# Optimization experiments

Measured on AMD Instinct MI355X. Metric: run time of the kernel, lower is better.

## Reference

```python
import jax, jax.numpy as jnp
import numpy as np

B, N, T = 2, 2048, 2048
ENC, DEC, HID = 1024, 1024, 1024
HEADS = 16
DH = HID // HEADS          # 64
HALF = DH // 2             # 32
LAMBDA_INIT = 0.8


def setup_inputs() -> dict:
    key = jax.random.key(0)
    ks = jax.random.split(key, 9)
    s = 0.02
    return {
        "encoder_feature": jax.random.normal(ks[0], (B, N, ENC), jnp.float32),
        "decoder_feature": jax.random.normal(ks[1], (B, T, DEC), jnp.float32),
        "Wq": jax.random.normal(ks[2], (HID, DEC), jnp.float32) * s,
        "Wk": jax.random.normal(ks[3], (HID, ENC), jnp.float32) * s,
        "Wv": jax.random.normal(ks[4], (HID, ENC), jnp.float32) * s,
        "lambda_q1": jax.random.normal(ks[5], (HALF,), jnp.float32) * 0.1,
        "lambda_q2": jax.random.normal(ks[6], (HALF,), jnp.float32) * 0.1,
        "lambda_k1": jax.random.normal(ks[7], (HALF,), jnp.float32) * 0.1,
        "lambda_k2": jax.random.normal(ks[8], (HALF,), jnp.float32) * 0.1,
    }


def reference(encoder_feature, decoder_feature, Wq, Wk, Wv,
              lambda_q1, lambda_q2, lambda_k1, lambda_k2):
    b, n, _ = encoder_feature.shape
    _, t, _ = decoder_feature.shape
    hid = Wq.shape[0]
    dh = hid // HEADS
    half = dh // 2

    q = decoder_feature @ Wq.T                                # [B,T,hid]
    k = encoder_feature @ Wk.T                                # [B,N,hid]
    v = encoder_feature @ Wv.T                                # [B,N,hid]

    q = q.reshape(b, t, 2 * HEADS, half).transpose(0, 2, 1, 3)  # [B,2H,T,half]
    k = k.reshape(b, n, 2 * HEADS, half).transpose(0, 2, 1, 3)  # [B,2H,N,half]
    v = v.reshape(b, n, HEADS, dh).transpose(0, 2, 1, 3)        # [B,H,N,dh]

    lam = (jnp.exp(jnp.sum(lambda_q1 * lambda_k1))
           - jnp.exp(jnp.sum(lambda_q2 * lambda_k2)) + LAMBDA_INIT)

    scale = 1.0 / jnp.sqrt(jnp.float32(half))
    att = jax.nn.softmax(jnp.einsum('bhtd,bhnd->bhtn', q, k) * scale, axis=-1)
    att = att.reshape(b, HEADS, 2, t, n)
    att = att[:, :, 0] - lam * att[:, :, 1]                   # [B,H,T,N]

    out = jnp.einsum('bhtn,bhnd->bhtd', att, v)               # [B,H,T,dh]
    return out.transpose(0, 2, 1, 3).reshape(b, t, hid)        # dropout: eval no-op
```

## Files before the change

### kernel.cpp

```cpp
#include <hip/hip_runtime.h>

typedef short bf16x8 __attribute__((ext_vector_type(8)));
typedef float f32x4  __attribute__((ext_vector_type(4)));
typedef unsigned int u32x2 __attribute__((ext_vector_type(2)));

#define B_SZ   2
#define T_SZ   2048
#define N_SZ   2048
#define HID_SZ 1024
#define NHEADS 16

#define SLOG2E 0.25500297f

static __device__ __forceinline__ float fexp2(float x) {
#if __has_builtin(__builtin_amdgcn_exp2f)
    return __builtin_amdgcn_exp2f(x);
#else
    float r; __asm__("v_exp_f32 %0, %1" : "=v"(r) : "v"(x)); return r;
#endif
}

static __device__ __forceinline__ short f2bf(float f) {
    unsigned u = __float_as_uint(f);
    u = (u + 0x7fffu + ((u >> 16) & 1u)) >> 16;
    return (short)u;
}

static __device__ __forceinline__ unsigned pk2(float a, float b) {
#if __has_builtin(__builtin_amdgcn_perm)
    return __builtin_amdgcn_perm(__float_as_uint(b) + 0x8000u,
                                 __float_as_uint(a) + 0x8000u, 0x07060302u);
#else
    unsigned ua = (__float_as_uint(a) + 0x8000u) >> 16;
    unsigned ub = (__float_as_uint(b) + 0x8000u) & 0xffff0000u;
    return ua | ub;
#endif
}

static __device__ __forceinline__ void gload16(const void* g, void* l) {
    __builtin_amdgcn_global_load_lds(
        (const __attribute__((address_space(1))) unsigned int*)g,
        (__attribute__((address_space(3))) unsigned int*)l, 16, 0, 0);
}

#define MFMA16(a, b, c) __builtin_amdgcn_mfma_f32_16x16x32_bf16((a), (b), (c), 0, 0, 0)

__global__ __launch_bounds__(256) void cvt_kernel(
    const float* __restrict__ dec, const float* __restrict__ enc,
    const float* __restrict__ Wq, const float* __restrict__ Wk,
    const float* __restrict__ Wv,
    short* __restrict__ decb, short* __restrict__ encb,
    short* __restrict__ wqb, short* __restrict__ wkb, short* __restrict__ wvb)
{
    const float* src; short* dst; int n;
    switch (blockIdx.y) {
      case 0: src = dec; dst = decb; n = B_SZ * T_SZ * HID_SZ; break;
      case 1: src = enc; dst = encb; n = B_SZ * N_SZ * HID_SZ; break;
      case 2: src = Wq;  dst = wqb;  n = HID_SZ * HID_SZ;      break;
      case 3: src = Wk;  dst = wkb;  n = HID_SZ * HID_SZ;      break;
      default:src = Wv;  dst = wvb;  n = HID_SZ * HID_SZ;      break;
    }
    const int idx = (blockIdx.x * 256 + threadIdx.x) * 8;
    if (idx >= n) return;
    float4 a = *(const float4*)&src[idx];
    float4 b = *(const float4*)&src[idx + 4];
    bf16x8 r;
    r[0]=f2bf(a.x); r[1]=f2bf(a.y); r[2]=f2bf(a.z); r[3]=f2bf(a.w);
    r[4]=f2bf(b.x); r[5]=f2bf(b.y); r[6]=f2bf(b.z); r[7]=f2bf(b.w);
    *(bf16x8*)&dst[idx] = r;
}

__global__ __launch_bounds__(256) void proj_kernel(
    const short* __restrict__ decb, const short* __restrict__ encb,
    const short* __restrict__ wqb, const short* __restrict__ wkb,
    const short* __restrict__ wvb,
    short* __restrict__ qbuf, short* __restrict__ kblk, short* __restrict__ vblk)
{
    const int i    = blockIdx.x;
    const int work = (i & 7) * 96 + (i >> 3);
    const int proj = work >> 8;
    const int rem  = work & 255;
    const int c0   = (rem >> 5) * 128;
    const int m0   = (rem & 31) * 128;

    const short* __restrict__ X = (proj == 0) ? decb : encb;
    const short* __restrict__ W = (proj == 0) ? wqb : ((proj == 1) ? wkb : wvb);

    __shared__ short As[128 * 64];
    __shared__ short Bs[128 * 64];

    const int tid  = threadIdx.x;
    const int lane = tid & 63;
    const int w    = tid >> 6;
    const int wm   = (w >> 1) * 64;
    const int wn   = (w & 1) * 64;
    const int q4   = lane >> 4;
    const int r16  = lane & 15;

    const int srow = w * 32;
    const int lrow = lane >> 3;
    const int lxor = (((lane & 7) ^ lrow) * 8);

    f32x4 acc[4][4] = {};

    for (int k0 = 0; k0 < HID_SZ; k0 += 64) {
        __syncthreads();
#pragma unroll
        for (int j = 0; j < 4; ++j) {
            const int row = srow + j * 8 + lrow;
            gload16(&X[(size_t)(m0 + row) * HID_SZ + k0 + lxor],
                    &As[(srow + j * 8) * 64]);
            gload16(&W[(size_t)(c0 + row) * HID_SZ + k0 + lxor],
                    &Bs[(srow + j * 8) * 64]);
        }
        __syncthreads();

#pragma unroll
        for (int kk = 0; kk < 2; ++kk) {
            bf16x8 af[4], bfr[4];
#pragma unroll
            for (int mi = 0; mi < 4; ++mi)
                af[mi] = *(const bf16x8*)&As[(wm + mi * 16 + r16) * 64
                                             + (((kk * 4 + q4) ^ (r16 & 7)) * 8)];
#pragma unroll
            for (int ni = 0; ni < 4; ++ni)
                bfr[ni] = *(const bf16x8*)&Bs[(wn + ni * 16 + r16) * 64
                                              + (((kk * 4 + q4) ^ (r16 & 7)) * 8)];
#pragma unroll
            for (int mi = 0; mi < 4; ++mi)
#pragma unroll
                for (int ni = 0; ni < 4; ++ni)
                    acc[mi][ni] = MFMA16(af[mi], bfr[ni], acc[mi][ni]);
        }
    }

#pragma unroll
    for (int mi = 0; mi < 4; ++mi)
#pragma unroll
    for (int ni = 0; ni < 4; ++ni)
#pragma unroll
    for (int r = 0; r < 4; ++r) {
        const int m = m0 + wm + mi * 16 + q4 * 4 + r;
        const int c = c0 + wn + ni * 16 + r16;
        const float v = acc[mi][ni][r];
        if (proj == 0) {
            qbuf[(size_t)m * HID_SZ + c] = f2bf(v * SLOG2E);
        } else {
            const int bb = m >> 11, n = m & (N_SZ - 1);
            const int hh = c >> 6;
            const int nc = n >> 6;
            const size_t base = ((size_t)((bb * NHEADS + hh) * 32 + nc)) * 4096;
            if (proj == 1) {
                const int row = n & 63, kd = c & 63;
                const int g = kd >> 3, e = kd & 7;
                kblk[base + row * 64 + (((g ^ (row & 7)) << 3) | e)] = f2bf(v);
            } else {
                const int vd = c & 63, nl = n & 63;
                const int np = ((nl & 15) << 2) | ((nl >> 4) & 3);
                const int g = np >> 3, e = np & 7;
                vblk[base + vd * 64 + (((g ^ (vd & 7)) << 3) | e)] = f2bf(v);
            }
        }
    }
}

__global__ __launch_bounds__(256) void attn_kernel(
    const short* __restrict__ qbuf, const short* __restrict__ kblk,
    const short* __restrict__ vblk,
    const float* __restrict__ lq1, const float* __restrict__ lq2,
    const float* __restrict__ lk1, const float* __restrict__ lk2,
    float* __restrict__ out)
{
    const int bi   = blockIdx.x;
    const int work = (bi & 7) * 128 + (bi >> 3);
    const int t0   = (work & 31) * 64;
    const int hb   = work >> 5;
    const int h    = hb & 15;
    const int b    = hb >> 4;

    const int tid = threadIdx.x;
    const int w    = tid >> 6;
    const int lane = tid & 63;
    const int q4   = lane >> 4;
    const int r16  = lane & 15;

    float d1 = 0.f, d2 = 0.f;
#pragma unroll
    for (int i = 0; i < 32; ++i) { d1 += lq1[i] * lk1[i]; d2 += lq2[i] * lk2[i]; }
    const float lam = __expf(d1) - __expf(d2) + 0.8f;

    __shared__ short Ks[4096];
    __shared__ short Vs[4096];
    __shared__ short Pl[4][2048];
    short* __restrict__ P = &Pl[w][0];

    const int trow = t0 + w * 16 + r16;
    const short* qrow = qbuf + ((size_t)(b * T_SZ + trow)) * HID_SZ + h * 64;
    const bf16x8 aq1 = *(const bf16x8*)(qrow + q4 * 8);
    const bf16x8 aq2 = *(const bf16x8*)(qrow + 32 + q4 * 8);

    const short* kbh = kblk + ((size_t)(b * NHEADS + h)) * 32 * 4096;
    const short* vbh = vblk + ((size_t)(b * NHEADS + h)) * 32 * 4096;

    bf16x8 ones;
#pragma unroll
    for (int i = 0; i < 8; ++i) ones[i] = (short)0x3F80;

    f32x4 o0[4] = {}, o1[4] = {};
    f32x4 l0a = {0.f, 0.f, 0.f, 0.f}, l1a = {0.f, 0.f, 0.f, 0.f};

    const int wg_half = (r16 >> 1);
    const int wlo     = (r16 & 1) * 4;
    const int swz     = r16 & 7;

    for (int nc = 0; nc < 32; ++nc) {
        const short* Kg = kbh + nc * 4096;
        const short* Vg = vbh + nc * 4096;

        __syncthreads();
#pragma unroll
        for (int j = 0; j < 2; ++j) {
            gload16(&Kg[(w * 2 + j) * 512 + lane * 8], &Ks[(w * 2 + j) * 512]);
            gload16(&Vg[(w * 2 + j) * 512 + lane * 8], &Vs[(w * 2 + j) * 512]);
        }
        __syncthreads();

        const f32x4 zz = {0.f, 0.f, 0.f, 0.f};
        f32x4 s0[4], s1[4];
#pragma unroll
        for (int s = 0; s < 4; ++s) {
            const int row = s * 16 + r16;
            bf16x8 bk1 = *(const bf16x8*)&Ks[row * 64 + ((q4 ^ swz) << 3)];
            bf16x8 bk2 = *(const bf16x8*)&Ks[row * 64 + (((4 + q4) ^ swz) << 3)];
            s0[s] = MFMA16(aq1, bk1, zz);
            s1[s] = MFMA16(aq2, bk2, zz);
        }

#pragma unroll
        for (int r = 0; r < 4; ++r) {
            const int row = q4 * 4 + r;
            const int wo  = row * 64 + ((wg_half ^ (row & 7)) << 3) + wlo;
            u32x2 pw;
            pw[0] = pk2(fexp2(s0[0][r]), fexp2(s0[1][r]));
            pw[1] = pk2(fexp2(s0[2][r]), fexp2(s0[3][r]));
            *(u32x2*)&P[wo] = pw;
            pw[0] = pk2(fexp2(s1[0][r]), fexp2(s1[1][r]));
            pw[1] = pk2(fexp2(s1[2][r]), fexp2(s1[3][r]));
            *(u32x2*)&P[1024 + wo] = pw;
        }

#pragma unroll
        for (int kk = 0; kk < 2; ++kk) {
            const int ro = r16 * 64 + (((kk * 4 + q4) ^ swz) << 3);
            bf16x8 ap0 = *(const bf16x8*)&P[ro];
            bf16x8 ap1 = *(const bf16x8*)&P[1024 + ro];
            l0a = MFMA16(ap0, ones, l0a);
            l1a = MFMA16(ap1, ones, l1a);
#pragma unroll
            for (int d = 0; d < 4; ++d) {
                const int vd = d * 16 + r16;
                bf16x8 bv = *(const bf16x8*)&Vs[vd * 64 + (((kk * 4 + q4) ^ swz) << 3)];
                o0[d] = MFMA16(ap0, bv, o0[d]);
                o1[d] = MFMA16(ap1, bv, o1[d]);
            }
        }
    }

    float rl0[4], rl1[4];
#pragma unroll
    for (int r = 0; r < 4; ++r) { rl0[r] = 1.f / l0a[r]; rl1[r] = lam / l1a[r]; }

#pragma unroll
    for (int d = 0; d < 4; ++d)
#pragma unroll
        for (int r = 0; r < 4; ++r) {
            const int t  = t0 + w * 16 + q4 * 4 + r;
            const int vd = d * 16 + r16;
            out[((size_t)(b * T_SZ + t)) * HID_SZ + h * 64 + vd] =
                o0[d][r] * rl0[r] - o1[d][r] * rl1[r];
        }
}

extern "C" void kernel_launch(void* const* d_in, const int* in_sizes, int n_in,
                              void* d_out, int out_size, void* d_ws, size_t ws_size,
                              hipStream_t stream)
{
    (void)in_sizes; (void)n_in; (void)out_size; (void)ws_size;

    const float* enc = (const float*)d_in[0];
    const float* dec = (const float*)d_in[1];
    const float* Wq  = (const float*)d_in[2];
    const float* Wk  = (const float*)d_in[3];
    const float* Wv  = (const float*)d_in[4];
    const float* lq1 = (const float*)d_in[5];
    const float* lq2 = (const float*)d_in[6];
    const float* lk1 = (const float*)d_in[7];
    const float* lk2 = (const float*)d_in[8];
    float* out = (float*)d_out;

    short* qbuf = (short*)d_ws;
    short* kblk = qbuf + (size_t)4096 * 1024;
    short* vblk = kblk + (size_t)4096 * 1024;
    short* decb = vblk + (size_t)4096 * 1024;
    short* encb = decb + (size_t)2 * 2048 * 1024;
    short* wqb  = encb + (size_t)2 * 2048 * 1024;
    short* wkb  = wqb  + (size_t)1024 * 1024;
    short* wvb  = wkb  + (size_t)1024 * 1024;

    cvt_kernel<<<dim3(2048, 5), 256, 0, stream>>>(
        dec, enc, Wq, Wk, Wv, decb, encb, wqb, wkb, wvb);

    proj_kernel<<<768, 256, 0, stream>>>(
        decb, encb, wqb, wkb, wvb, qbuf, kblk, vblk);

    attn_kernel<<<1024, 256, 0, stream>>>(
        qbuf, kblk, vblk, lq1, lq2, lk1, lk2, out);
}
```

Measured before the change: 245.7 us.

## Software-pipeline projection GEMM loads and double-buffer K/V tiles in attention

The projection GEMM now prefetches the next K-slice from global memory into registers while MFMAs run on the current shared tile, then stores it to LDS. The attention kernel double-buffers K/V chunks in shared memory, issuing async loads for chunk nc+1 before computing chunk nc, which drops one barrier per iteration. The P scratch buffer is halved by processing the two softmax halves sequentially and reusing the loaded V fragments. This is meant to hide global-load latency, at the cost of more registers and more LDS for the K/V buffers. One risk: the single barrier at the top of each attention iteration may not guarantee that the async gload16 of chunk nc+1 has landed before the next iteration reads it.

Result: slower. 319.0 us (+29.8%).

```diff
diff --git a/kernel.cpp b/kernel.cpp
--- a/kernel.cpp
+++ b/kernel.cpp
@@ -101,19 +101,40 @@
     const int lrow = lane >> 3;
     const int lxor = (((lane & 7) ^ lrow) * 8);
 
+    size_t gx[4], gw[4];
+    int ldso[4];
+#pragma unroll
+    for (int j = 0; j < 4; ++j) {
+        const int row = srow + j * 8 + lrow;
+        gx[j] = (size_t)(m0 + row) * HID_SZ + lxor;
+        gw[j] = (size_t)(c0 + row) * HID_SZ + lxor;
+        ldso[j] = (srow + j * 8) * 64 + lane * 8;
+    }
+
+    uint4 ra[4], rb[4];
+#pragma unroll
+    for (int j = 0; j < 4; ++j) {
+        ra[j] = *(const uint4*)&X[gx[j]];
+        rb[j] = *(const uint4*)&W[gw[j]];
+    }
+#pragma unroll
+    for (int j = 0; j < 4; ++j) {
+        *(uint4*)&As[ldso[j]] = ra[j];
+        *(uint4*)&Bs[ldso[j]] = rb[j];
+    }
+    __syncthreads();
+
     f32x4 acc[4][4] = {};
 
-    for (int k0 = 0; k0 < HID_SZ; k0 += 64) {
-        __syncthreads();
-#pragma unroll
-        for (int j = 0; j < 4; ++j) {
-            const int row = srow + j * 8 + lrow;
-            gload16(&X[(size_t)(m0 + row) * HID_SZ + k0 + lxor],
-                    &As[(srow + j * 8) * 64]);
-            gload16(&W[(size_t)(c0 + row) * HID_SZ + k0 + lxor],
-                    &Bs[(srow + j * 8) * 64]);
-        }
-        __syncthreads();
+    for (int it = 0; it < 16; ++it) {
+        if (it < 15) {
+            const int k1 = (it + 1) * 64;
+#pragma unroll
+            for (int j = 0; j < 4; ++j) {
+                ra[j] = *(const uint4*)&X[gx[j] + k1];
+                rb[j] = *(const uint4*)&W[gw[j] + k1];
+            }
+        }
 
 #pragma unroll
         for (int kk = 0; kk < 2; ++kk) {
@@ -131,6 +152,16 @@
 #pragma unroll
                 for (int ni = 0; ni < 4; ++ni)
                     acc[mi][ni] = MFMA16(af[mi], bfr[ni], acc[mi][ni]);
+        }
+
+        if (it < 15) {
+            __syncthreads();
+#pragma unroll
+            for (int j = 0; j < 4; ++j) {
+                *(uint4*)&As[ldso[j]] = ra[j];
+                *(uint4*)&Bs[ldso[j]] = rb[j];
+            }
+            __syncthreads();
         }
     }
 
@@ -189,9 +220,8 @@
     for (int i = 0; i < 32; ++i) { d1 += lq1[i] * lk1[i]; d2 += lq2[i] * lk2[i]; }
     const float lam = __expf(d1) - __expf(d2) + 0.8f;
 
-    __shared__ short Ks[4096];
-    __shared__ short Vs[4096];
-    __shared__ short Pl[4][2048];
+    __shared__ short KV[2][8192];
+    __shared__ short Pl[4][1024];
     short* __restrict__ P = &Pl[w][0];
 
     const int trow = t0 + w * 16 + r16;
@@ -213,17 +243,30 @@
     const int wlo     = (r16 & 1) * 4;
     const int swz     = r16 & 7;
 
+#pragma unroll
+    for (int j = 0; j < 2; ++j) {
+        gload16(&kbh[(w * 2 + j) * 512 + lane * 8], &KV[0][(w * 2 + j) * 512]);
+        gload16(&vbh[(w * 2 + j) * 512 + lane * 8], &KV[0][4096 + (w * 2 + j) * 512]);
+    }
+
     for (int nc = 0; nc < 32; ++nc) {
-        const short* Kg = kbh + nc * 4096;
-        const short* Vg = vbh + nc * 4096;
-
+        const int cur = nc & 1;
         __syncthreads();
-#pragma unroll
-        for (int j = 0; j < 2; ++j) {
-            gload16(&Kg[(w * 2 + j) * 512 + lane * 8], &Ks[(w * 2 + j) * 512]);
-            gload16(&Vg[(w * 2 + j) * 512 + lane * 8], &Vs[(w * 2 + j) * 512]);
-        }
-        __syncthreads();
+
+        if (nc + 1 < 32) {
+            const short* Kg = kbh + (nc + 1) * 4096;
+            const short* Vg = vbh + (nc + 1) * 4096;
+#pragma unroll
+            for (int j = 0; j < 2; ++j) {
+                gload16(&Kg[(w * 2 + j) * 512 + lane * 8],
+                        &KV[cur ^ 1][(w * 2 + j) * 512]);
+                gload16(&Vg[(w * 2 + j) * 512 + lane * 8],
+                        &KV[cur ^ 1][4096 + (w * 2 + j) * 512]);
+            }
+        }
+
+        const short* Ks = &KV[cur][0];
+        const short* Vs = &KV[cur][4096];
 
         const f32x4 zz = {0.f, 0.f, 0.f, 0.f};
         f32x4 s0[4], s1[4];
@@ -235,6 +278,8 @@
             s0[s] = MFMA16(aq1, bk1, zz);
             s1[s] = MFMA16(aq2, bk2, zz);
         }
+
+        bf16x8 vv[2][4];
 
 #pragma unroll
         for (int r = 0; r < 4; ++r) {
@@ -244,25 +289,37 @@
             pw[0] = pk2(fexp2(s0[0][r]), fexp2(s0[1][r]));
             pw[1] = pk2(fexp2(s0[2][r]), fexp2(s0[3][r]));
             *(u32x2*)&P[wo] = pw;
+        }
+#pragma unroll
+        for (int kk = 0; kk < 2; ++kk) {
+            const int ro = r16 * 64 + (((kk * 4 + q4) ^ swz) << 3);
+            bf16x8 ap = *(const bf16x8*)&P[ro];
+            l0a = MFMA16(ap, ones, l0a);
+#pragma unroll
+            for (int d = 0; d < 4; ++d) {
+                vv[kk][d] = *(const bf16x8*)&Vs[(d * 16 + r16) * 64
+                                                + (((kk * 4 + q4) ^ swz) << 3)];
+                o0[d] = MFMA16(ap, vv[kk][d], o0[d]);
+            }
+        }
+
+#pragma unroll
+        for (int r = 0; r < 4; ++r) {
+            const int row = q4 * 4 + r;
+            const int wo  = row * 64 + ((wg_half ^ (row & 7)) << 3) + wlo;
+            u32x2 pw;
             pw[0] = pk2(fexp2(s1[0][r]), fexp2(s1[1][r]));
             pw[1] = pk2(fexp2(s1[2][r]), fexp2(s1[3][r]));
-            *(u32x2*)&P[1024 + wo] = pw;
-        }
-
+            *(u32x2*)&P[wo] = pw;
+        }
 #pragma unroll
         for (int kk = 0; kk < 2; ++kk) {
             const int ro = r16 * 64 + (((kk * 4 + q4) ^ swz) << 3);
-            bf16x8 ap0 = *(const bf16x8*)&P[ro];
-            bf16x8 ap1 = *(const bf16x8*)&P[1024 + ro];
-            l0a = MFMA16(ap0, ones, l0a);
-            l1a = MFMA16(ap1, ones, l1a);
-#pragma unroll
-            for (int d = 0; d < 4; ++d) {
-                const int vd = d * 16 + r16;
-                bf16x8 bv = *(const bf16x8*)&Vs[vd * 64 + (((kk * 4 + q4) ^ swz) << 3)];
-                o0[d] = MFMA16(ap0, bv, o0[d]);
-                o1[d] = MFMA16(ap1, bv, o1[d]);
-            }
+            bf16x8 ap = *(const bf16x8*)&P[ro];
+            l1a = MFMA16(ap, ones, l1a);
+#pragma unroll
+            for (int d = 0; d < 4; ++d)
+                o1[d] = MFMA16(ap, vv[kk][d], o1[d]);
         }
     }
 
```
